# Kernel optimization log

Hardware: AMD Instinct MI355X
Metric: run time of the kernel (lower is better)

The kernel has to match this reference:

```python
import jax, jax.numpy as jnp
import numpy as np

B, L, D, H, E, K = 2, 2048, 1024, 2048, 8, 2
NOISE_EPS = 0.01
CVLOSS, SWITCHLOSS, ZLOSS = 0.01, 0.1, 0.0001


def setup_inputs() -> dict:
    key = jax.random.key(0)
    k0, k1, k2, k3, k4 = jax.random.split(key, 5)
    x = jax.random.normal(k0, (B, L, D), jnp.float32)
    # gating weight (torch zero-inits; use small random so routing is nontrivial)
    w_gate = jax.random.normal(k1, (D, 2 * E), jnp.float32) * 0.02
    w1 = jax.random.normal(k2, (E, D, H), jnp.float32) * (1.0 / np.sqrt(D))
    w2 = jax.random.normal(k3, (E, H, D), jnp.float32) * (1.0 / np.sqrt(H))
    eps = jax.random.normal(k4, (B * L, E), jnp.float32)  # gating noise (randn_like)
    return {"x": x, "w_gate": w_gate, "w1": w1, "w2": w2, "eps": eps}


def moe_forward(x, w_gate, w1, w2, eps):
    b, l, d = x.shape
    T = b * l
    xf = x.reshape(T, d)                                   # [T, D]
    # --- noisy top-k gating ---
    clean, raw = jnp.split(xf @ w_gate, 2, axis=-1)        # each [T, E]
    noise_stddev = jax.nn.softplus(raw) + NOISE_EPS
    logits = clean + eps * noise_stddev
    probs = jax.nn.softmax(logits, axis=1)                 # [T, E]
    top_g, top_i = jax.lax.top_k(probs, K)                 # [T, K]
    rows = jnp.arange(T)[:, None]
    gates = jnp.zeros_like(probs).at[rows, top_i].set(top_g)  # dense gates [T, E]
    # --- aux losses (acc_aux_loss path disabled in source) ---
    expert_size = (gates > 0).sum(0).astype(jnp.float32)   # tokens per expert [E]
    g_sum = gates.sum(0)
    g_norm = g_sum / g_sum.sum()                           # F.normalize p=1
    cv = jnp.var(g_norm, ddof=1) / (jnp.mean(g_norm) ** 2 + 1e-10)  # torch unbiased var
    p_norm = probs.sum(0) / probs.sum()
    f_norm = expert_size / expert_size.sum()
    switch = (1.0 - (p_norm * f_norm).sum()) * E
    zl = jnp.mean(jax.nn.logsumexp(logits, axis=1) ** 2)
    loss = CVLOSS * cv + SWITCHLOSS * switch + ZLOSS * zl
    # --- expert compute + gated combine (grouped GEMM expressed as batched einsum;
    #     gates are zero off the top-k so math matches sort/dispatch/index_add) ---
    h = jax.nn.relu(jnp.einsum('td,edh->teh', xf, w1))     # [T, E, H]
    out = jnp.einsum('teh,ehd->ted', h, w2)                # [T, E, D]
    y = jnp.einsum('ted,te->td', out, gates)               # combine, multiply_by_gates
    return y.reshape(b, l, d), loss


def reference(x, w_gate, w1, w2, eps):
    return moe_forward(x, w_gate, w1, w2, eps)
```

## Files before the change

### kernel.cpp

```cpp
#include <hip/hip_runtime.h>

#define TT 4096
#define DD 1024
#define HH 2048
#define EE 8
#define TK 8192

typedef short  bf16x8 __attribute__((ext_vector_type(8)));
typedef float  f32x4  __attribute__((ext_vector_type(4)));

__device__ __forceinline__ unsigned short f2b(float f) {
    unsigned int u = __float_as_uint(f);
    unsigned int r = (u + 0x7fffu + ((u >> 16) & 1u)) >> 16;
    return (unsigned short)r;
}
__device__ __forceinline__ float b2f(unsigned short b) {
    return __uint_as_float(((unsigned int)b) << 16);
}

#define GLOAD_LDS16(SRC, DST) __builtin_amdgcn_global_load_lds( \
    (const __attribute__((address_space(1))) unsigned int*)(SRC), \
    (__attribute__((address_space(3))) unsigned int*)(DST), 16, 0, 0)

__global__ __launch_bounds__(256) void convw(
    const float* __restrict__ w1, const float* __restrict__ w2,
    unsigned short* __restrict__ w1bT, unsigned short* __restrict__ w2bT) {
    int b = blockIdx.x;
    const float* src; unsigned short* dst; int Kd, Nd, lb;
    if (b < 1024) { src = w1; dst = w1bT; Kd = 1024; Nd = 2048; lb = b; }
    else          { src = w2; dst = w2bT; Kd = 2048; Nd = 1024; lb = b - 1024; }
    int nx = Nd >> 7, ny = Kd >> 7;
    int bx = lb % nx, by = (lb / nx) % ny, e = lb / (nx * ny);
    int n0 = bx * 128, k0 = by * 128;
    const float* s = src + (size_t)e * Kd * Nd;
    unsigned short* d = dst + (size_t)e * Kd * Nd;
    __shared__ float tile[128][129];
    int rg = threadIdx.x >> 5;
    int c4 = (threadIdx.x & 31) * 4;
#pragma unroll
    for (int i = 0; i < 16; i++) {
        int r = rg + i * 8;
        float4 v = *(const float4*)(s + (size_t)(k0 + r) * Nd + n0 + c4);
        tile[r][c4 + 0] = v.x; tile[r][c4 + 1] = v.y;
        tile[r][c4 + 2] = v.z; tile[r][c4 + 3] = v.w;
    }
    __syncthreads();
#pragma unroll
    for (int i = 0; i < 16; i++) {
        int n = rg + i * 8;
        ushort4 o;
        o.x = f2b(tile[c4 + 0][n]);
        o.y = f2b(tile[c4 + 1][n]);
        o.z = f2b(tile[c4 + 2][n]);
        o.w = f2b(tile[c4 + 3][n]);
        *(ushort4*)(d + (size_t)(n0 + n) * Kd + k0 + c4) = o;
    }
}

__global__ __launch_bounds__(256) void gating(
    const float* __restrict__ x, const float* __restrict__ wg, const float* __restrict__ eps,
    float* __restrict__ stats_f, int* __restrict__ stats_i,
    int* __restrict__ top_i, float* __restrict__ top_g,
    unsigned short* __restrict__ xb) {
    __shared__ float l_psum[8], l_gsum[8], l_zl;
    __shared__ int   l_cr[8], l_cp[8];
    int tid = threadIdx.x;
    if (tid < 8) { l_psum[tid] = 0.f; l_gsum[tid] = 0.f; l_cr[tid] = 0; l_cp[tid] = 0; }
    if (tid == 0) l_zl = 0.f;
    __syncthreads();
    int wave = tid >> 6, lane = tid & 63;
    int t = blockIdx.x * 4 + wave;
    const float* xr = x + (size_t)t * DD;
    unsigned short* xbr = xb + (size_t)t * DD;
#pragma unroll
    for (int i = 0; i < 4; i++) {
        int idx = lane + i * 64;
        float4 v = ((const float4*)xr)[idx];
        ushort4 o;
        o.x = f2b(v.x); o.y = f2b(v.y); o.z = f2b(v.z); o.w = f2b(v.w);
        ((ushort4*)xbr)[idx] = o;
    }
    int sub = lane >> 2, part = lane & 3;
    float a0 = 0.f, a1 = 0.f, a2 = 0.f, a3 = 0.f;
#pragma unroll 8
    for (int i = 0; i < 64; i++) {
        int dd = sub + i * 16;
        float xv = xr[dd];
        float4 w4 = *(const float4*)(wg + dd * 16 + part * 4);
        a0 += xv * w4.x; a1 += xv * w4.y; a2 += xv * w4.z; a3 += xv * w4.w;
    }
#pragma unroll
    for (int o = 4; o < 64; o <<= 1) {
        a0 += __shfl_xor(a0, o, 64);
        a1 += __shfl_xor(a1, o, 64);
        a2 += __shfl_xor(a2, o, 64);
        a3 += __shfl_xor(a3, o, 64);
    }
    float f16v[16];
#pragma unroll
    for (int src2 = 0; src2 < 4; src2++) {
        f16v[src2 * 4 + 0] = __shfl(a0, src2, 64);
        f16v[src2 * 4 + 1] = __shfl(a1, src2, 64);
        f16v[src2 * 4 + 2] = __shfl(a2, src2, 64);
        f16v[src2 * 4 + 3] = __shfl(a3, src2, 64);
    }
    if (lane == 0) {
        float lg[8], p[8];
        float mx = -1e30f;
        for (int e2 = 0; e2 < 8; e2++) {
            float raw = f16v[8 + e2];
            float sp = (raw > 20.f) ? raw : log1pf(__expf(raw));
            float l = f16v[e2] + eps[(size_t)t * 8 + e2] * (sp + 0.01f);
            lg[e2] = l; mx = fmaxf(mx, l);
        }
        float se = 0.f;
        for (int e2 = 0; e2 < 8; e2++) { p[e2] = __expf(lg[e2] - mx); se += p[e2]; }
        float lse = mx + logf(se);
        float inv = 1.f / se;
        for (int e2 = 0; e2 < 8; e2++) p[e2] *= inv;
        int i0 = 0;
        for (int e2 = 1; e2 < 8; e2++) if (p[e2] > p[i0]) i0 = e2;
        int i1 = (i0 == 0) ? 1 : 0;
        for (int e2 = 0; e2 < 8; e2++) if (e2 != i0 && p[e2] > p[i1]) i1 = e2;
        float g0 = p[i0], g1 = p[i1];
        top_i[t * 2] = i0; top_i[t * 2 + 1] = i1;
        top_g[t * 2] = g0; top_g[t * 2 + 1] = g1;
        for (int e2 = 0; e2 < 8; e2++) atomicAdd(&l_psum[e2], p[e2]);
        atomicAdd(&l_gsum[i0], g0); atomicAdd(&l_gsum[i1], g1);
        atomicAdd(&l_zl, lse * lse);
        atomicAdd(&l_cr[i0], 1); atomicAdd(&l_cr[i1], 1);
        if (g0 > 0.f) atomicAdd(&l_cp[i0], 1);
        if (g1 > 0.f) atomicAdd(&l_cp[i1], 1);
    }
    __syncthreads();
    if (tid < 8) {
        atomicAdd(&stats_f[tid],      l_psum[tid]);
        atomicAdd(&stats_f[8 + tid],  l_gsum[tid]);
        atomicAdd(&stats_i[tid],      l_cr[tid]);
        atomicAdd(&stats_i[8 + tid],  l_cp[tid]);
    }
    if (tid == 0) atomicAdd(&stats_f[16], l_zl);
}

__global__ void scatter(const int* __restrict__ top_i, int* __restrict__ stats_i,
                        const float* __restrict__ stats_f,
                        int* __restrict__ row_token, int* __restrict__ pair_pos,
                        float* __restrict__ loss_out) {
    __shared__ int lcnt[8], lbase[8], soffs[9];
    int tid = threadIdx.x;
    if (tid < 8) lcnt[tid] = 0;
    if (tid == 0) {
        int off = 0;
        for (int e = 0; e < 8; e++) { soffs[e] = off; off += stats_i[e]; }
        soffs[8] = off;
    }
    __syncthreads();
    int t = blockIdx.x * 256 + tid;
    int e0 = top_i[t * 2], e1 = top_i[t * 2 + 1];
    int p0 = atomicAdd(&lcnt[e0], 1);
    int p1 = atomicAdd(&lcnt[e1], 1);
    __syncthreads();
    if (tid < 8) lbase[tid] = atomicAdd(&stats_i[16 + tid], lcnt[tid]);
    __syncthreads();
    int idx0 = soffs[e0] + lbase[e0] + p0;
    int idx1 = soffs[e1] + lbase[e1] + p1;
    row_token[idx0] = t;
    row_token[idx1] = t;
    pair_pos[t * 2] = idx0;
    pair_pos[t * 2 + 1] = idx1;
    if (blockIdx.x == 0 && tid == 0) {
        for (int e = 0; e < 9; e++) stats_i[24 + e] = soffs[e];
        float gs = 0.f;
        for (int e = 0; e < 8; e++) gs += stats_f[8 + e];
        float var = 0.f;
        for (int e = 0; e < 8; e++) {
            float gn = stats_f[8 + e] / gs;
            float d = gn - 0.125f;
            var += d * d;
        }
        var /= 7.f;
        float cv = var / (0.015625f + 1e-10f);
        float ps = 0.f, cs = 0.f;
        for (int e = 0; e < 8; e++) { ps += stats_f[e]; cs += (float)stats_i[8 + e]; }
        float dot = 0.f;
        for (int e = 0; e < 8; e++) dot += (stats_f[e] / ps) * ((float)stats_i[8 + e] / cs);
        float sw = (1.f - dot) * 8.f;
        float zl = stats_f[16] / (float)TT;
        *loss_out = 0.01f * cv + 0.1f * sw + 0.0001f * zl;
    }
}

template<int KTOT, int KSPLITS, int NTILES, bool GATHER, bool RELU>
__global__ __launch_bounds__(512, 1) void gemm_mt(
    const unsigned short* __restrict__ A,
    const unsigned short* __restrict__ Bt,
    unsigned short* __restrict__ C, long long split_stride,
    const int* __restrict__ row_token, const int* __restrict__ stats_i) {
    constexpr int KD   = KTOT / KSPLITS;
    constexpr int NK   = KD / 64;
    constexpr int NI   = NK / 2;
    constexpr int NDIM = NTILES * 256;
    static_assert(NTILES * KSPLITS == 8, "q must span 8");

    __shared__ __align__(16) unsigned short Al[2 * 256 * 64];
    __shared__ __align__(16) unsigned short Bl[2 * 256 * 64];

    const int* offs = stats_i + 24;
    int tid = threadIdx.x;
    int lane = tid & 63, wave = tid >> 6;

    if (blockIdx.x < 256) {
        int lin = blockIdx.x;
        int e   = lin & 7;
        int rem = lin >> 3;
        int q4  = rem & 7;
        int rt  = rem >> 3;
        int n0  = (q4 % NTILES) * 256;
        int split = q4 / NTILES;
        int off = offs[e];
        int ne  = offs[e + 1] - off;
        if (rt * 256 >= ne) return;

        int wm = wave >> 2, wn = wave & 3;

        const unsigned short* Asrc[4];
#pragma unroll
        for (int i = 0; i < 4; i++) {
            int glin = i * 512 + tid, row = glin >> 3, sl = glin & 7, g = sl ^ (row & 7);
            int arow;
            if (GATHER) arow = row_token[min(off + rt * 256 + row, TK - 1)];
            else        arow = min(off + rt * 256 + row, TK - 1);
            Asrc[i] = A + (size_t)arow * KTOT + split * KD + g * 8;
        }
        const unsigned short* Bte = Bt + (size_t)e * NDIM * KTOT;
        const unsigned short* Bsrc[4];
#pragma unroll
        for (int i = 0; i < 4; i++) {
            int glin = i * 512 + tid, row = glin >> 3, sl = glin & 7, g = sl ^ (row & 7);
            Bsrc[i] = Bte + (size_t)(n0 + row) * KTOT + split * KD + g * 8;
        }

        f32x4 acc[8][4];
#pragma unroll
        for (int m = 0; m < 8; m++)
#pragma unroll
            for (int n = 0; n < 4; n++)
#pragma unroll
                for (int i = 0; i < 4; i++) acc[m][n][i] = 0.f;

        bf16x8 bv[2][4], av[2][2];

#define STG_A(SLOT, KT, CC) GLOAD_LDS16(Asrc[CC] + (KT) * 64, Al + (SLOT) * 16384 + (CC) * 4096 + wave * 512)
#define STG_B(SLOT, KT, CC) GLOAD_LDS16(Bsrc[CC] + (KT) * 64, Bl + (SLOT) * 16384 + (CC) * 4096 + wave * 512)

#define LOAD_B(SLOT) do { \
    _Pragma("unroll") for (int kk2 = 0; kk2 < 2; kk2++) \
    _Pragma("unroll") for (int n = 0; n < 4; n++) { \
        int row = wn * 64 + n * 16 + (lane & 15); \
        int g = (kk2 * 4 + (lane >> 4)) ^ (row & 7); \
        bv[kk2][n] = *(const bf16x8*)(Bl + (SLOT) * 16384 + row * 64 + g * 8); \
    } } while (0)

#define LOAD_AQ(SLOT, QQ) do { \
    _Pragma("unroll") for (int kk2 = 0; kk2 < 2; kk2++) \
    _Pragma("unroll") for (int mi = 0; mi < 2; mi++) { \
        int row = wm * 128 + (QQ) * 32 + mi * 16 + (lane & 15); \
        int g = (kk2 * 4 + (lane >> 4)) ^ (row & 7); \
        av[kk2][mi] = *(const bf16x8*)(Al + (SLOT) * 16384 + row * 64 + g * 8); \
    } } while (0)

#define MFMA_Q(QQ) do { \
    _Pragma("unroll") for (int kk2 = 0; kk2 < 2; kk2++) \
    _Pragma("unroll") for (int mi = 0; mi < 2; mi++) \
    _Pragma("unroll") for (int n = 0; n < 4; n++) \
        acc[(QQ) * 2 + mi][n] = __builtin_amdgcn_mfma_f32_16x16x32_bf16(av[kk2][mi], bv[kk2][n], acc[(QQ) * 2 + mi][n], 0, 0, 0); \
    } while (0)

#define PHASE(SLOT, QQ, STAGE_STMT, WAIT_STMT) do { \
    if ((QQ) == 0) LOAD_B(SLOT); \
    LOAD_AQ(SLOT, QQ); \
    STAGE_STMT; \
    __builtin_amdgcn_s_barrier(); \
    asm volatile("s_waitcnt lgkmcnt(0)" ::: "memory"); \
    __builtin_amdgcn_s_setprio(1); \
    MFMA_Q(QQ); \
    __builtin_amdgcn_s_setprio(0); \
    WAIT_STMT; \
    __builtin_amdgcn_s_barrier(); \
    } while (0)

#pragma unroll
        for (int c = 0; c < 4; c++) STG_B(0, 0, c);
#pragma unroll
        for (int c = 0; c < 4; c++) STG_A(0, 0, c);
#pragma unroll
        for (int c = 0; c < 4; c++) STG_B(1, 1, c);
        STG_A(1, 1, 0); STG_A(1, 1, 2);
        asm volatile("s_waitcnt vmcnt(6)" ::: "memory");
        __builtin_amdgcn_s_barrier();

#pragma unroll 1
        for (int it = 0; it < NI; ++it) {
            int u = 2 * it, v = u + 1;
            bool ns = (it + 1 < NI);
            PHASE(0, 0, { STG_A(1, v, 1); STG_A(1, v, 3); }, {});
            PHASE(0, 1, { if (ns) { STG_B(0, u + 2, 0); STG_B(0, u + 2, 1); } }, {});
            PHASE(0, 2, { if (ns) { STG_B(0, u + 2, 2); STG_B(0, u + 2, 3); } }, {});
            PHASE(0, 3, { if (ns) { STG_A(0, u + 2, 0); STG_A(0, u + 2, 2); } },
                        { if (ns) asm volatile("s_waitcnt vmcnt(6)" ::: "memory");
                          else    asm volatile("s_waitcnt vmcnt(0)" ::: "memory"); });
            PHASE(1, 0, { if (ns) { STG_A(0, u + 2, 1); STG_A(0, u + 2, 3); } }, {});
            PHASE(1, 1, { if (ns) { STG_B(1, v + 2, 0); STG_B(1, v + 2, 1); } }, {});
            PHASE(1, 2, { if (ns) { STG_B(1, v + 2, 2); STG_B(1, v + 2, 3); } }, {});
            PHASE(1, 3, { if (ns) { STG_A(1, v + 2, 0); STG_A(1, v + 2, 2); } },
                        { if (ns) asm volatile("s_waitcnt vmcnt(6)" ::: "memory"); });
        }
#undef PHASE
#undef MFMA_Q
#undef LOAD_AQ
#undef LOAD_B
#undef STG_A
#undef STG_B

        unsigned short* Cb = C + (ptrdiff_t)split * split_stride;
#pragma unroll
        for (int m = 0; m < 8; m++) {
            int rr0 = rt * 256 + wm * 128 + m * 16 + (lane >> 4) * 4;
#pragma unroll
            for (int i = 0; i < 4; i++) {
                if (rr0 + i < ne) {
                    size_t grow = (size_t)(off + rr0 + i);
#pragma unroll
                    for (int n = 0; n < 4; n++) {
                        int col = n0 + wn * 64 + n * 16 + (lane & 15);
                        float vvv = acc[m][n][i];
                        if (RELU) vvv = fmaxf(vvv, 0.f);
                        Cb[grow * NDIM + col] = f2b(vvv);
                    }
                }
            }
        }
    } else {
        int t   = blockIdx.x - 256;
        int e   = t & 7;
        int rem = t >> 3;
        int q4  = rem & 7;
        int s   = rem >> 3;
        int n0  = (q4 % NTILES) * 256;
        int split = q4 / NTILES;
        int off = offs[e];
        int ne  = offs[e + 1] - off;
        int m0  = 1024 + s * 64;
        if (m0 >= ne) return;

        int wm = wave >> 2, wn = wave & 3;

        const unsigned short* Asrc;
        {
            int row = tid >> 3, sl = tid & 7, g = sl ^ (row & 7);
            int arow;
            if (GATHER) arow = row_token[min(off + m0 + row, TK - 1)];
            else        arow = min(off + m0 + row, TK - 1);
            Asrc = A + (size_t)arow * KTOT + split * KD + g * 8;
        }
        const unsigned short* Bte = Bt + (size_t)e * NDIM * KTOT;
        const unsigned short* Bsrc[4];
#pragma unroll
        for (int i = 0; i < 4; i++) {
            int glin = i * 512 + tid, row = glin >> 3, sl = glin & 7, g = sl ^ (row & 7);
            Bsrc[i] = Bte + (size_t)(n0 + row) * KTOT + split * KD + g * 8;
        }

        f32x4 acc2[2][4];
#pragma unroll
        for (int m = 0; m < 2; m++)
#pragma unroll
            for (int n = 0; n < 4; n++)
#pragma unroll
                for (int i = 0; i < 4; i++) acc2[m][n][i] = 0.f;

#define TSTG(BUF, KT) do { \
    GLOAD_LDS16(Asrc + (KT) * 64, Al + (BUF) * 4096 + wave * 512); \
    _Pragma("unroll") for (int c_ = 0; c_ < 4; c_++) \
        GLOAD_LDS16(Bsrc[c_] + (KT) * 64, Bl + (BUF) * 16384 + c_ * 4096 + wave * 512); \
} while (0)

        TSTG(0, 0);
        asm volatile("s_waitcnt vmcnt(0)" ::: "memory");
        __builtin_amdgcn_s_barrier();

#pragma unroll 1
        for (int kt = 0; kt < NK; ++kt) {
            if (kt + 1 < NK) TSTG((kt & 1) ^ 1, kt + 1);
            int B = kt & 1;
            bf16x8 a2[2][2], b2[2][4];
#pragma unroll
            for (int kk2 = 0; kk2 < 2; kk2++) {
#pragma unroll
                for (int mi = 0; mi < 2; mi++) {
                    int row = wm * 32 + mi * 16 + (lane & 15);
                    int g = (kk2 * 4 + (lane >> 4)) ^ (row & 7);
                    a2[kk2][mi] = *(const bf16x8*)(Al + B * 4096 + row * 64 + g * 8);
                }
#pragma unroll
                for (int n = 0; n < 4; n++) {
                    int row = wn * 64 + n * 16 + (lane & 15);
                    int g = (kk2 * 4 + (lane >> 4)) ^ (row & 7);
                    b2[kk2][n] = *(const bf16x8*)(Bl + B * 16384 + row * 64 + g * 8);
                }
            }
#pragma unroll
            for (int kk2 = 0; kk2 < 2; kk2++)
#pragma unroll
                for (int mi = 0; mi < 2; mi++)
#pragma unroll
                    for (int n = 0; n < 4; n++)
                        acc2[mi][n] = __builtin_amdgcn_mfma_f32_16x16x32_bf16(a2[kk2][mi], b2[kk2][n], acc2[mi][n], 0, 0, 0);
            asm volatile("s_waitcnt vmcnt(0) lgkmcnt(0)" ::: "memory");
            __builtin_amdgcn_s_barrier();
        }
#undef TSTG

        unsigned short* Cb = C + (ptrdiff_t)split * split_stride;
#pragma unroll
        for (int mi = 0; mi < 2; mi++) {
            int rr0 = m0 + wm * 32 + mi * 16 + (lane >> 4) * 4;
#pragma unroll
            for (int i = 0; i < 4; i++) {
                if (rr0 + i < ne) {
                    size_t grow = (size_t)(off + rr0 + i);
#pragma unroll
                    for (int n = 0; n < 4; n++) {
                        int col = n0 + wn * 64 + n * 16 + (lane & 15);
                        float vvv = acc2[mi][n][i];
                        if (RELU) vvv = fmaxf(vvv, 0.f);
                        Cb[grow * NDIM + col] = f2b(vvv);
                    }
                }
            }
        }
    }
}

__global__ void combine(const unsigned short* __restrict__ o0,
                        const unsigned short* __restrict__ o1,
                        const int* __restrict__ pair_pos, const float* __restrict__ top_g,
                        float* __restrict__ y) {
    int t = blockIdx.x;
    int tid = threadIdx.x;
    int i0 = pair_pos[t * 2], i1 = pair_pos[t * 2 + 1];
    float g0 = top_g[t * 2], g1 = top_g[t * 2 + 1];
    int d0 = tid * 4;
    ushort4 a0 = *(const ushort4*)(o0 + (size_t)i0 * DD + d0);
    ushort4 a1 = *(const ushort4*)(o1 + (size_t)i0 * DD + d0);
    ushort4 b0 = *(const ushort4*)(o0 + (size_t)i1 * DD + d0);
    ushort4 b1 = *(const ushort4*)(o1 + (size_t)i1 * DD + d0);
    float4 o;
    o.x = g0 * (b2f(a0.x) + b2f(a1.x)) + g1 * (b2f(b0.x) + b2f(b1.x));
    o.y = g0 * (b2f(a0.y) + b2f(a1.y)) + g1 * (b2f(b0.y) + b2f(b1.y));
    o.z = g0 * (b2f(a0.z) + b2f(a1.z)) + g1 * (b2f(b0.z) + b2f(b1.z));
    o.w = g0 * (b2f(a0.w) + b2f(a1.w)) + g1 * (b2f(b0.w) + b2f(b1.w));
    *(float4*)(y + (size_t)t * DD + d0) = o;
}

extern "C" void kernel_launch(void* const* d_in, const int* in_sizes, int n_in,
                              void* d_out, int out_size, void* d_ws, size_t ws_size,
                              hipStream_t stream) {
    const float* x   = (const float*)d_in[0];
    const float* wg  = (const float*)d_in[1];
    const float* w1  = (const float*)d_in[2];
    const float* w2  = (const float*)d_in[3];
    const float* eps = (const float*)d_in[4];
    float* y = (float*)d_out;
    char* ws = (char*)d_ws;

    unsigned short* xb    = (unsigned short*)(ws);
    unsigned short* w1bT  = (unsigned short*)(ws + 8388608);
    unsigned short* w2bT  = (unsigned short*)(ws + 41943040);
    unsigned short* hbuf  = (unsigned short*)(ws + 75497472);
    unsigned short* outp0 = (unsigned short*)(ws + 109051904);
    unsigned short* outp1 = (unsigned short*)(ws + 8388608);
    int*   top_i    = (int*)(ws + 125829120);
    float* top_g    = (float*)(ws + 125861888);
    int*   row_token= (int*)(ws + 125894656);
    int*   pair_pos = (int*)(ws + 125927424);
    float* stats_f  = (float*)(ws + 125960192);
    int*   stats_i  = (int*)(ws + 125960192 + 128);

    hipMemsetAsync(ws + 125960192, 0, 768, stream);
    gating<<<1024, 256, 0, stream>>>(x, wg, eps, stats_f, stats_i, top_i, top_g, xb);
    convw<<<2048, 256, 0, stream>>>(w1, w2, w1bT, w2bT);
    scatter<<<16, 256, 0, stream>>>(top_i, stats_i, stats_f, row_token, pair_pos, y + (size_t)TT * DD);
    gemm_mt<1024, 1, 8, true,  true ><<<512, 512, 0, stream>>>(
        xb, w1bT, hbuf, 0, row_token, stats_i);
    gemm_mt<2048, 2, 4, false, false><<<512, 512, 0, stream>>>(
        hbuf, w2bT, outp0, (long long)(outp1 - outp0), row_token, stats_i);
    combine<<<4096, 256, 0, stream>>>(outp0, outp1, pair_pos, top_g, y);
}
```

Before: 199.0 us.

## Merge gating and weight conversion into one launch; triple-buffer tail GEMM loads

```diff
diff --git a/kernel.cpp b/kernel.cpp
--- a/kernel.cpp
+++ b/kernel.cpp
@@ -22,124 +22,124 @@
     (const __attribute__((address_space(1))) unsigned int*)(SRC), \
     (__attribute__((address_space(3))) unsigned int*)(DST), 16, 0, 0)
 
-__global__ __launch_bounds__(256) void convw(
+__global__ __launch_bounds__(256) void prep2(
     const float* __restrict__ w1, const float* __restrict__ w2,
-    unsigned short* __restrict__ w1bT, unsigned short* __restrict__ w2bT) {
-    int b = blockIdx.x;
-    const float* src; unsigned short* dst; int Kd, Nd, lb;
-    if (b < 1024) { src = w1; dst = w1bT; Kd = 1024; Nd = 2048; lb = b; }
-    else          { src = w2; dst = w2bT; Kd = 2048; Nd = 1024; lb = b - 1024; }
-    int nx = Nd >> 7, ny = Kd >> 7;
-    int bx = lb % nx, by = (lb / nx) % ny, e = lb / (nx * ny);
-    int n0 = bx * 128, k0 = by * 128;
-    const float* s = src + (size_t)e * Kd * Nd;
-    unsigned short* d = dst + (size_t)e * Kd * Nd;
-    __shared__ float tile[128][129];
-    int rg = threadIdx.x >> 5;
-    int c4 = (threadIdx.x & 31) * 4;
-#pragma unroll
-    for (int i = 0; i < 16; i++) {
-        int r = rg + i * 8;
-        float4 v = *(const float4*)(s + (size_t)(k0 + r) * Nd + n0 + c4);
-        tile[r][c4 + 0] = v.x; tile[r][c4 + 1] = v.y;
-        tile[r][c4 + 2] = v.z; tile[r][c4 + 3] = v.w;
-    }
-    __syncthreads();
-#pragma unroll
-    for (int i = 0; i < 16; i++) {
-        int n = rg + i * 8;
-        ushort4 o;
-        o.x = f2b(tile[c4 + 0][n]);
-        o.y = f2b(tile[c4 + 1][n]);
-        o.z = f2b(tile[c4 + 2][n]);
-        o.w = f2b(tile[c4 + 3][n]);
-        *(ushort4*)(d + (size_t)(n0 + n) * Kd + k0 + c4) = o;
-    }
-}
-
-__global__ __launch_bounds__(256) void gating(
+    unsigned short* __restrict__ w1bT, unsigned short* __restrict__ w2bT,
     const float* __restrict__ x, const float* __restrict__ wg, const float* __restrict__ eps,
     float* __restrict__ stats_f, int* __restrict__ stats_i,
     int* __restrict__ top_i, float* __restrict__ top_g,
     unsigned short* __restrict__ xb) {
-    __shared__ float l_psum[8], l_gsum[8], l_zl;
-    __shared__ int   l_cr[8], l_cp[8];
-    int tid = threadIdx.x;
-    if (tid < 8) { l_psum[tid] = 0.f; l_gsum[tid] = 0.f; l_cr[tid] = 0; l_cp[tid] = 0; }
-    if (tid == 0) l_zl = 0.f;
-    __syncthreads();
-    int wave = tid >> 6, lane = tid & 63;
-    int t = blockIdx.x * 4 + wave;
-    const float* xr = x + (size_t)t * DD;
-    unsigned short* xbr = xb + (size_t)t * DD;
-#pragma unroll
-    for (int i = 0; i < 4; i++) {
-        int idx = lane + i * 64;
-        float4 v = ((const float4*)xr)[idx];
-        ushort4 o;
-        o.x = f2b(v.x); o.y = f2b(v.y); o.z = f2b(v.z); o.w = f2b(v.w);
-        ((ushort4*)xbr)[idx] = o;
+    __shared__ float tile[128][129];
+    int b = blockIdx.x;
+    if (b < 2048) {
+        const float* src; unsigned short* dst; int Kd, Nd, lb;
+        if (b < 1024) { src = w1; dst = w1bT; Kd = 1024; Nd = 2048; lb = b; }
+        else          { src = w2; dst = w2bT; Kd = 2048; Nd = 1024; lb = b - 1024; }
+        int nx = Nd >> 7, ny = Kd >> 7;
+        int bx = lb % nx, by = (lb / nx) % ny, e = lb / (nx * ny);
+        int n0 = bx * 128, k0 = by * 128;
+        const float* s = src + (size_t)e * Kd * Nd;
+        unsigned short* d = dst + (size_t)e * Kd * Nd;
+        int rg = threadIdx.x >> 5;
+        int c4 = (threadIdx.x & 31) * 4;
+#pragma unroll
+        for (int i = 0; i < 16; i++) {
+            int r = rg + i * 8;
+            float4 v = *(const float4*)(s + (size_t)(k0 + r) * Nd + n0 + c4);
+            tile[r][c4 + 0] = v.x; tile[r][c4 + 1] = v.y;
+            tile[r][c4 + 2] = v.z; tile[r][c4 + 3] = v.w;
+        }
+        __syncthreads();
+#pragma unroll
+        for (int i = 0; i < 16; i++) {
+            int n = rg + i * 8;
+            ushort4 o;
+            o.x = f2b(tile[c4 + 0][n]);
+            o.y = f2b(tile[c4 + 1][n]);
+            o.z = f2b(tile[c4 + 2][n]);
+            o.w = f2b(tile[c4 + 3][n]);
+            *(ushort4*)(d + (size_t)(n0 + n) * Kd + k0 + c4) = o;
+        }
+    } else {
+        __shared__ float l_psum[8], l_gsum[8], l_zl;
+        __shared__ int   l_cr[8], l_cp[8];
+        int tid = threadIdx.x;
+        if (tid < 8) { l_psum[tid] = 0.f; l_gsum[tid] = 0.f; l_cr[tid] = 0; l_cp[tid] = 0; }
+        if (tid == 0) l_zl = 0.f;
+        __syncthreads();
+        int wave = tid >> 6, lane = tid & 63;
+        int t = (b - 2048) * 4 + wave;
+        const float* xr = x + (size_t)t * DD;
+        unsigned short* xbr = xb + (size_t)t * DD;
+#pragma unroll
+        for (int i = 0; i < 4; i++) {
+            int idx = lane + i * 64;
+            float4 v = ((const float4*)xr)[idx];
+            ushort4 o;
+            o.x = f2b(v.x); o.y = f2b(v.y); o.z = f2b(v.z); o.w = f2b(v.w);
+            ((ushort4*)xbr)[idx] = o;
+        }
+        int sub = lane >> 2, part = lane & 3;
+        float a0 = 0.f, a1 = 0.f, a2 = 0.f, a3 = 0.f;
+#pragma unroll 8
+        for (int i = 0; i < 64; i++) {
+            int dd = sub + i * 16;
+            float xv = xr[dd];
+            float4 w4 = *(const float4*)(wg + dd * 16 + part * 4);
+            a0 += xv * w4.x; a1 += xv * w4.y; a2 += xv * w4.z; a3 += xv * w4.w;
+        }
+#pragma unroll
+        for (int o = 4; o < 64; o <<= 1) {
+            a0 += __shfl_xor(a0, o, 64);
+            a1 += __shfl_xor(a1, o, 64);
+            a2 += __shfl_xor(a2, o, 64);
+            a3 += __shfl_xor(a3, o, 64);
+        }
+        float f16v[16];
+#pragma unroll
+        for (int src2 = 0; src2 < 4; src2++) {
+            f16v[src2 * 4 + 0] = __shfl(a0, src2, 64);
+            f16v[src2 * 4 + 1] = __shfl(a1, src2, 64);
+            f16v[src2 * 4 + 2] = __shfl(a2, src2, 64);
+            f16v[src2 * 4 + 3] = __shfl(a3, src2, 64);
+        }
+        if (lane == 0) {
+            float lg[8], p[8];
+            float mx = -1e30f;
+            for (int e2 = 0; e2 < 8; e2++) {
+                float raw = f16v[8 + e2];
+                float sp = (raw > 20.f) ? raw : log1pf(__expf(raw));
+                float l = f16v[e2] + eps[(size_t)t * 8 + e2] * (sp + 0.01f);
+                lg[e2] = l; mx = fmaxf(mx, l);
+            }
+            float se = 0.f;
+            for (int e2 = 0; e2 < 8; e2++) { p[e2] = __expf(lg[e2] - mx); se += p[e2]; }
+            float lse = mx + logf(se);
+            float inv = 1.f / se;
+            for (int e2 = 0; e2 < 8; e2++) p[e2] *= inv;
+            int i0 = 0;
+            for (int e2 = 1; e2 < 8; e2++) if (p[e2] > p[i0]) i0 = e2;
+            int i1 = (i0 == 0) ? 1 : 0;
+            for (int e2 = 0; e2 < 8; e2++) if (e2 != i0 && p[e2] > p[i1]) i1 = e2;
+            float g0 = p[i0], g1 = p[i1];
+            top_i[t * 2] = i0; top_i[t * 2 + 1] = i1;
+            top_g[t * 2] = g0; top_g[t * 2 + 1] = g1;
+            for (int e2 = 0; e2 < 8; e2++) atomicAdd(&l_psum[e2], p[e2]);
+            atomicAdd(&l_gsum[i0], g0); atomicAdd(&l_gsum[i1], g1);
+            atomicAdd(&l_zl, lse * lse);
+            atomicAdd(&l_cr[i0], 1); atomicAdd(&l_cr[i1], 1);
+            if (g0 > 0.f) atomicAdd(&l_cp[i0], 1);
+            if (g1 > 0.f) atomicAdd(&l_cp[i1], 1);
+        }
+        __syncthreads();
+        if (tid < 8) {
+            atomicAdd(&stats_f[tid],      l_psum[tid]);
+            atomicAdd(&stats_f[8 + tid],  l_gsum[tid]);
+            atomicAdd(&stats_i[tid],      l_cr[tid]);
+            atomicAdd(&stats_i[8 + tid],  l_cp[tid]);
+        }
+        if (tid == 0) atomicAdd(&stats_f[16], l_zl);
     }
-    int sub = lane >> 2, part = lane & 3;
-    float a0 = 0.f, a1 = 0.f, a2 = 0.f, a3 = 0.f;
-#pragma unroll 8
-    for (int i = 0; i < 64; i++) {
-        int dd = sub + i * 16;
-        float xv = xr[dd];
-        float4 w4 = *(const float4*)(wg + dd * 16 + part * 4);
-        a0 += xv * w4.x; a1 += xv * w4.y; a2 += xv * w4.z; a3 += xv * w4.w;
-    }
-#pragma unroll
-    for (int o = 4; o < 64; o <<= 1) {
-        a0 += __shfl_xor(a0, o, 64);
-        a1 += __shfl_xor(a1, o, 64);
-        a2 += __shfl_xor(a2, o, 64);
-        a3 += __shfl_xor(a3, o, 64);
-    }
-    float f16v[16];
-#pragma unroll
-    for (int src2 = 0; src2 < 4; src2++) {
-        f16v[src2 * 4 + 0] = __shfl(a0, src2, 64);
-        f16v[src2 * 4 + 1] = __shfl(a1, src2, 64);
-        f16v[src2 * 4 + 2] = __shfl(a2, src2, 64);
-        f16v[src2 * 4 + 3] = __shfl(a3, src2, 64);
-    }
-    if (lane == 0) {
-        float lg[8], p[8];
-        float mx = -1e30f;
-        for (int e2 = 0; e2 < 8; e2++) {
-            float raw = f16v[8 + e2];
-            float sp = (raw > 20.f) ? raw : log1pf(__expf(raw));
-            float l = f16v[e2] + eps[(size_t)t * 8 + e2] * (sp + 0.01f);
-            lg[e2] = l; mx = fmaxf(mx, l);
-        }
-        float se = 0.f;
-        for (int e2 = 0; e2 < 8; e2++) { p[e2] = __expf(lg[e2] - mx); se += p[e2]; }
-        float lse = mx + logf(se);
-        float inv = 1.f / se;
-        for (int e2 = 0; e2 < 8; e2++) p[e2] *= inv;
-        int i0 = 0;
-        for (int e2 = 1; e2 < 8; e2++) if (p[e2] > p[i0]) i0 = e2;
-        int i1 = (i0 == 0) ? 1 : 0;
-        for (int e2 = 0; e2 < 8; e2++) if (e2 != i0 && p[e2] > p[i1]) i1 = e2;
-        float g0 = p[i0], g1 = p[i1];
-        top_i[t * 2] = i0; top_i[t * 2 + 1] = i1;
-        top_g[t * 2] = g0; top_g[t * 2 + 1] = g1;
-        for (int e2 = 0; e2 < 8; e2++) atomicAdd(&l_psum[e2], p[e2]);
-        atomicAdd(&l_gsum[i0], g0); atomicAdd(&l_gsum[i1], g1);
-        atomicAdd(&l_zl, lse * lse);
-        atomicAdd(&l_cr[i0], 1); atomicAdd(&l_cr[i1], 1);
-        if (g0 > 0.f) atomicAdd(&l_cp[i0], 1);
-        if (g1 > 0.f) atomicAdd(&l_cp[i1], 1);
-    }
-    __syncthreads();
-    if (tid < 8) {
-        atomicAdd(&stats_f[tid],      l_psum[tid]);
-        atomicAdd(&stats_f[8 + tid],  l_gsum[tid]);
-        atomicAdd(&stats_i[tid],      l_cr[tid]);
-        atomicAdd(&stats_i[8 + tid],  l_cp[tid]);
-    }
-    if (tid == 0) atomicAdd(&stats_f[16], l_zl);
 }
 
 __global__ void scatter(const int* __restrict__ top_i, int* __restrict__ stats_i,
@@ -345,12 +345,12 @@
         int e   = t & 7;
         int rem = t >> 3;
         int q4  = rem & 7;
-        int s   = rem >> 3;
+        int s0  = rem >> 3;
         int n0  = (q4 % NTILES) * 256;
         int split = q4 / NTILES;
         int off = offs[e];
         int ne  = offs[e + 1] - off;
-        int m0  = 1024 + s * 64;
+        int m0  = 1024 + s0 * 64;
         if (m0 >= ne) return;
 
         int wm = wave >> 2, wn = wave & 3;
@@ -379,20 +379,25 @@
 #pragma unroll
                 for (int i = 0; i < 4; i++) acc2[m][n][i] = 0.f;
 
-#define TSTG(BUF, KT) do { \
-    GLOAD_LDS16(Asrc + (KT) * 64, Al + (BUF) * 4096 + wave * 512); \
+#define TTSG(S, KT) do { \
+    unsigned short* Ab_ = Al + (S) * 4096; \
+    unsigned short* Bb_ = ((S) == 2) ? (Al + 16384) : (Bl + (S) * 16384); \
+    GLOAD_LDS16(Asrc + (KT) * 64, Ab_ + wave * 512); \
     _Pragma("unroll") for (int c_ = 0; c_ < 4; c_++) \
-        GLOAD_LDS16(Bsrc[c_] + (KT) * 64, Bl + (BUF) * 16384 + c_ * 4096 + wave * 512); \
+        GLOAD_LDS16(Bsrc[c_] + (KT) * 64, Bb_ + c_ * 4096 + wave * 512); \
 } while (0)
 
-        TSTG(0, 0);
-        asm volatile("s_waitcnt vmcnt(0)" ::: "memory");
-        __builtin_amdgcn_s_barrier();
-
+        TTSG(0, 0);
+        TTSG(1, 1);
+        int sb = 0;
 #pragma unroll 1
         for (int kt = 0; kt < NK; ++kt) {
-            if (kt + 1 < NK) TSTG((kt & 1) ^ 1, kt + 1);
-            int B = kt & 1;
+            if (kt + 1 < NK) asm volatile("s_waitcnt vmcnt(5)" ::: "memory");
+            else             asm volatile("s_waitcnt vmcnt(0)" ::: "memory");
+            __builtin_amdgcn_s_barrier();
+            if (kt + 2 < NK) { int s2 = sb + 2; if (s2 >= 3) s2 -= 3; TTSG(s2, kt + 2); }
+            const unsigned short* Ab = Al + sb * 4096;
+            const unsigned short* Bb = (sb == 2) ? (Al + 16384) : (Bl + sb * 16384);
             bf16x8 a2[2][2], b2[2][4];
 #pragma unroll
             for (int kk2 = 0; kk2 < 2; kk2++) {
@@ -400,13 +405,13 @@
                 for (int mi = 0; mi < 2; mi++) {
                     int row = wm * 32 + mi * 16 + (lane & 15);
                     int g = (kk2 * 4 + (lane >> 4)) ^ (row & 7);
-                    a2[kk2][mi] = *(const bf16x8*)(Al + B * 4096 + row * 64 + g * 8);
+                    a2[kk2][mi] = *(const bf16x8*)(Ab + row * 64 + g * 8);
                 }
 #pragma unroll
                 for (int n = 0; n < 4; n++) {
                     int row = wn * 64 + n * 16 + (lane & 15);
                     int g = (kk2 * 4 + (lane >> 4)) ^ (row & 7);
-                    b2[kk2][n] = *(const bf16x8*)(Bl + B * 16384 + row * 64 + g * 8);
+                    b2[kk2][n] = *(const bf16x8*)(Bb + row * 64 + g * 8);
                 }
             }
 #pragma unroll
@@ -416,10 +421,9 @@
 #pragma unroll
                     for (int n = 0; n < 4; n++)
                         acc2[mi][n] = __builtin_amdgcn_mfma_f32_16x16x32_bf16(a2[kk2][mi], b2[kk2][n], acc2[mi][n], 0, 0, 0);
-            asm volatile("s_waitcnt vmcnt(0) lgkmcnt(0)" ::: "memory");
-            __builtin_amdgcn_s_barrier();
-        }
-#undef TSTG
+            sb = (sb == 2) ? 0 : sb + 1;
+        }
+#undef TTSG
 
         unsigned short* Cb = C + (ptrdiff_t)split * split_stride;
 #pragma unroll
@@ -488,8 +492,8 @@
     int*   stats_i  = (int*)(ws + 125960192 + 128);
 
     hipMemsetAsync(ws + 125960192, 0, 768, stream);
-    gating<<<1024, 256, 0, stream>>>(x, wg, eps, stats_f, stats_i, top_i, top_g, xb);
-    convw<<<2048, 256, 0, stream>>>(w1, w2, w1bT, w2bT);
+    prep2<<<3072, 256, 0, stream>>>(w1, w2, w1bT, w2bT, x, wg, eps,
+                                    stats_f, stats_i, top_i, top_g, xb);
     scatter<<<16, 256, 0, stream>>>(top_i, stats_i, stats_f, row_token, pair_pos, y + (size_t)TT * DD);
     gemm_mt<1024, 1, 8, true,  true ><<<512, 512, 0, stream>>>(
         xb, w1bT, hbuf, 0, row_token, stats_i);
```

Result: faster. 190.6 us (-4.3%).
